# Kernel tuning notes

Measured on AMD Instinct MI355X. Metric: run time of the kernel, lower is better.

## Reference

```python
import jax, jax.numpy as jnp
import numpy as np

B, C, H, W = 8, 256, 56, 56
CI = 64  # inter_channels = C // reduction


def setup_inputs() -> dict:
    key = jax.random.key(0)
    ks = jax.random.split(key, 8)
    s = 0.05
    return {
        "x": jax.random.normal(ks[0], (B, C, H, W), jnp.float32),
        "Wq": jax.random.normal(ks[1], (CI, C), jnp.float32) * s,
        "bq": jax.random.normal(ks[2], (CI,), jnp.float32) * s,
        "Wk": jax.random.normal(ks[3], (CI, C), jnp.float32) * s,
        "bk": jax.random.normal(ks[4], (CI,), jnp.float32) * s,
        "Wv": jax.random.normal(ks[5], (C, C), jnp.float32) * s,
        "bv": jax.random.normal(ks[6], (C,), jnp.float32) * s,
        "gamma": jax.random.normal(ks[7], (1,), jnp.float32) * s,
    }


def reference(x, Wq, bq, Wk, bk, Wv, bv, gamma):
    b, c, h, w = x.shape
    n = h * w
    xf = x.reshape(b, c, n)  # [B, C, N]
    # 1x1 convs == per-pixel linear projections
    q = jnp.einsum('oc,bcn->bno', Wq, xf) + bq          # [B, N, CI]
    k = jnp.einsum('oc,bcn->bon', Wk, xf) + bk[:, None]  # [B, CI, N]
    score = jnp.einsum('bno,bom->bnm', q, k)             # [B, N, N] (no scaling, as in source)
    attention = jax.nn.softmax(score, axis=-1)
    v = jnp.einsum('oc,bcn->bon', Wv, xf) + bv[:, None]  # [B, C, N]
    # out[b,c,i] = sum_j v[b,c,j] * attention[b,i,j]  (== bmm(V, att^T))
    out = jnp.einsum('bcj,bij->bci', v, attention).reshape(b, c, h, w)
    return gamma[0] * out + x
```

## Files before the change

### kernel.cpp

```cpp
#include <hip/hip_runtime.h>


constexpr int B_  = 8;
constexpr int C_  = 256;
constexpr int CI_ = 64;
constexpr int N_  = 3136;
constexpr int JS  = 4;
constexpr int JT  = 32;
constexpr int VSP = 40;
constexpr int PN  = 64;
constexpr int XSP = C_ + 8;

typedef __attribute__((ext_vector_type(8))) short short8;
typedef __attribute__((ext_vector_type(4))) float f32x4;
typedef __attribute__((ext_vector_type(4))) ushort us4;

static __device__ inline ushort f2b(float f) {
    unsigned u = __float_as_uint(f);
    return (ushort)((u + 0x7fffu + ((u >> 16) & 1u)) >> 16);
}
static __device__ inline float b2f(ushort h) {
    return __uint_as_float(((unsigned)h) << 16);
}

__global__ __launch_bounds__(256)
void pre_kernel(const float* __restrict__ x,
                const float* __restrict__ Wq, const float* __restrict__ Wk,
                const float* __restrict__ Wv,
                ushort* __restrict__ xT, ushort* __restrict__ wqk, ushort* __restrict__ wv)
{
    __shared__ float ts[64][65];
    const int bx  = blockIdx.x;
    const int tid = threadIdx.x;

    if (bx >= B_ * 196) {
        int i = (bx - B_ * 196) * 256 + tid;
        if (i < 16384)      wqk[i] = f2b(Wq[i]);
        else if (i < 32768) wqk[i] = f2b(Wk[i - 16384]);
        wv[i] = f2b(Wv[i]);
        return;
    }

    const int b  = bx / 196;
    const int rm = bx % 196;
    const int n0 = (rm >> 2) * 64;
    const int c0 = (rm & 3) * 64;

    const float* src = x + ((size_t)b * C_ + c0) * N_ + n0;
    #pragma unroll
    for (int rep = 0; rep < 16; rep++) {
        int e = rep * 256 + tid;
        int c = e >> 6, n = e & 63;
        ts[c][n] = src[(size_t)c * N_ + n];
    }
    __syncthreads();
    ushort* dst = xT + ((size_t)b * N_ + n0) * C_ + c0;
    #pragma unroll
    for (int rep = 0; rep < 8; rep++) {
        int e = rep * 256 + tid;
        int n = e >> 5, c2 = (e & 31) * 2;
        ushort2 o;
        o.x = f2b(ts[c2][n]);
        o.y = f2b(ts[c2 + 1][n]);
        *(ushort2*)(dst + (size_t)n * C_ + c2) = o;
    }
}

__global__ __launch_bounds__(256)
void proj_kernel(const ushort* __restrict__ xT, const ushort* __restrict__ wqk,
                 const ushort* __restrict__ wv,
                 const float* __restrict__ bq, const float* __restrict__ bk,
                 const float* __restrict__ bv,
                 ushort* __restrict__ qb, ushort* __restrict__ kb, ushort* __restrict__ vt)
{
    __shared__ ushort xs[PN][XSP];
    const int b   = blockIdx.x / 49;
    const int n0  = (blockIdx.x % 49) * PN;
    const int tid = threadIdx.x;
    const int w    = tid >> 6;
    const int lane = tid & 63;
    const int m16  = lane & 15;
    const int quad = lane >> 4;

    {
        const ushort* src = xT + ((size_t)b * N_ + n0) * C_;
        #pragma unroll
        for (int rep = 0; rep < 8; rep++) {
            int e = rep * 256 + tid;
            int row = e >> 5, ch = (e & 31) * 8;
            *(short8*)&xs[row][ch] = *(const short8*)(src + (size_t)row * C_ + ch);
        }
    }
    __syncthreads();

    {
        f32x4 acc[2][4];
        #pragma unroll
        for (int mt = 0; mt < 2; mt++)
            #pragma unroll
            for (int nt = 0; nt < 4; nt++) acc[mt][nt] = (f32x4){0.f, 0.f, 0.f, 0.f};

        #pragma unroll
        for (int kk = 0; kk < 8; kk++) {
            short8 af[2];
            #pragma unroll
            for (int mt = 0; mt < 2; mt++)
                af[mt] = *(const short8*)(wqk + (size_t)(w * 32 + mt * 16 + m16) * C_ + kk * 32 + quad * 8);
            #pragma unroll
            for (int nt = 0; nt < 4; nt++) {
                short8 bf = *(const short8*)&xs[nt * 16 + m16][kk * 32 + quad * 8];
                #pragma unroll
                for (int mt = 0; mt < 2; mt++)
                    acc[mt][nt] = __builtin_amdgcn_mfma_f32_16x16x32_bf16(af[mt], bf, acc[mt][nt], 0, 0, 0);
            }
        }
        const float* bias = (w < 2) ? bq : bk;
        ushort* dst = (w < 2) ? qb : kb;
        const int obase = (w & 1) * 32;
        #pragma unroll
        for (int mt = 0; mt < 2; mt++) {
            f32x4 bs = *(const f32x4*)(bias + obase + mt * 16 + quad * 4);
            #pragma unroll
            for (int nt = 0; nt < 4; nt++) {
                us4 pk;
                pk.x = f2b(acc[mt][nt][0] + bs[0]);
                pk.y = f2b(acc[mt][nt][1] + bs[1]);
                pk.z = f2b(acc[mt][nt][2] + bs[2]);
                pk.w = f2b(acc[mt][nt][3] + bs[3]);
                *(us4*)(dst + ((size_t)b * N_ + n0 + nt * 16 + m16) * CI_ + obase + mt * 16 + quad * 4) = pk;
            }
        }
    }

    {
        f32x4 vacc[4][4];
        #pragma unroll
        for (int mt = 0; mt < 4; mt++)
            #pragma unroll
            for (int nt = 0; nt < 4; nt++) vacc[mt][nt] = (f32x4){0.f, 0.f, 0.f, 0.f};

        #pragma unroll
        for (int kk = 0; kk < 8; kk++) {
            short8 af[4];
            #pragma unroll
            for (int mt = 0; mt < 4; mt++)
                af[mt] = *(const short8*)&xs[mt * 16 + m16][kk * 32 + quad * 8];
            #pragma unroll
            for (int nt = 0; nt < 4; nt++) {
                short8 bf = *(const short8*)(wv + (size_t)(w * 64 + nt * 16 + m16) * C_ + kk * 32 + quad * 8);
                #pragma unroll
                for (int mt = 0; mt < 4; mt++)
                    vacc[mt][nt] = __builtin_amdgcn_mfma_f32_16x16x32_bf16(af[mt], bf, vacc[mt][nt], 0, 0, 0);
            }
        }
        #pragma unroll
        for (int nt = 0; nt < 4; nt++) {
            int c = w * 64 + nt * 16 + m16;
            float bvc = bv[c];
            #pragma unroll
            for (int mt = 0; mt < 4; mt++) {
                us4 pk;
                pk.x = f2b(vacc[mt][nt][0] + bvc);
                pk.y = f2b(vacc[mt][nt][1] + bvc);
                pk.z = f2b(vacc[mt][nt][2] + bvc);
                pk.w = f2b(vacc[mt][nt][3] + bvc);
                *(us4*)(vt + ((size_t)b * C_ + c) * N_ + n0 + mt * 16 + quad * 4) = pk;
            }
        }
    }
}

__global__ __launch_bounds__(256, 2)
void attn_kernel(const ushort* __restrict__ qb, const ushort* __restrict__ kb,
                 const ushort* __restrict__ vt,
                 ushort* __restrict__ op, float* __restrict__ lp)
{
    __shared__ __align__(16) ushort vs[2][C_][VSP];

    const int bx   = blockIdx.x;
    const int b    = bx & 7;
    const int rem  = bx >> 3;
    const int t    = rem >> 2;
    const int js   = rem & 3;
    const int tid  = threadIdx.x;
    const int w    = tid >> 6;
    const int lane = tid & 63;
    const int m16  = lane & 15;
    const int quad = lane >> 4;
    const int i0   = t * 64 + w * 16;

    const int steps = (js == 0) ? 13 : 12;
    const int jbase = ((js == 0) ? 0 : (1 + 12 * js)) * JT;

    const ushort* vtb = vt + (size_t)b * C_ * N_;
    const ushort* kbb = kb + (size_t)b * N_ * CI_;

    short8 qf[2];
    {
        const ushort* qbase = qb + ((size_t)b * N_ + i0 + m16) * CI_;
        qf[0] = *(const short8*)(qbase + quad * 8);
        qf[1] = *(const short8*)(qbase + 32 + quad * 8);
    }

    f32x4 O[16];
    #pragma unroll
    for (int ct = 0; ct < 16; ct++) O[ct] = (f32x4){0.f, 0.f, 0.f, 0.f};
    float lsum = 0.f;

    const int sc  = tid >> 2;
    const int seg = tid & 3;
    const int p0  = (seg & 1) * 16 + (seg >> 1) * 4;

    short8 prA[4], prB[4];
    short8 krA[4], krB[4];

    #define PREFETCH(PR, J0)                                                   \
        {                                                                      \
            _Pragma("unroll")                                                  \
            for (int p = 0; p < 4; p++)                                        \
                PR[p] = *(const short8*)(vtb + (size_t)(p * 64 + sc) * N_ + (J0) + seg * 8); \
        }
    #define COMMIT(PR, BUF)                                                    \
        {                                                                      \
            _Pragma("unroll")                                                  \
            for (int p = 0; p < 4; p++) {                                      \
                *(us4*)&vs[BUF][p * 64 + sc][p0]     = ((const us4*)&PR[p])[0]; \
                *(us4*)&vs[BUF][p * 64 + sc][p0 + 8] = ((const us4*)&PR[p])[1]; \
            }                                                                  \
        }
    #define KLOAD(J0, KR)                                                      \
        {                                                                      \
            _Pragma("unroll")                                                  \
            for (int h = 0; h < 2; h++) {                                      \
                const ushort* krow = kbb + (size_t)((J0) + h * 16 + m16) * CI_; \
                KR[2 * h]     = *(const short8*)(krow + quad * 8);             \
                KR[2 * h + 1] = *(const short8*)(krow + 32 + quad * 8);        \
            }                                                                  \
        }
    #define BAR()                                                              \
        {                                                                      \
            __builtin_amdgcn_sched_barrier(0);                                 \
            asm volatile("s_waitcnt lgkmcnt(0)");                              \
            __builtin_amdgcn_sched_barrier(0);                                 \
            __builtin_amdgcn_s_barrier();                                      \
            __builtin_amdgcn_sched_barrier(0);                                 \
        }

    PREFETCH(prA, jbase)
    PREFETCH(prB, jbase + JT)
    KLOAD(jbase, krA)
    COMMIT(prA, 0)
    BAR()

    #define STEP(CUR, PRC, PRN, KRC, KRN, ST)                                  \
    {                                                                          \
        const int j0_ = jbase + (ST) * JT;                                     \
        const bool more1_ = (ST) + 1 < steps;                                  \
        if ((ST) + 2 < steps) PREFETCH(PRN, j0_ + 2 * JT)                      \
        if (more1_) KLOAD(j0_ + JT, KRN)                                       \
                      \
        short8 pa;                                                             \
        _Pragma("unroll")                                                      \
        for (int h = 0; h < 2; h++) {                                          \
            f32x4 T = (f32x4){0.f, 0.f, 0.f, 0.f};                             \
            T = __builtin_amdgcn_mfma_f32_16x16x32_bf16(KRC[2 * h],     qf[0], T, 0, 0, 0); \
            T = __builtin_amdgcn_mfma_f32_16x16x32_bf16(KRC[2 * h + 1], qf[1], T, 0, 0, 0); \
            _Pragma("unroll")                                                  \
            for (int r = 0; r < 4; r++) {                                      \
                float pv = __expf(T[r] - 12.0f);             \
                lsum += pv;                                                    \
                pa[h * 4 + r] = (short)f2b(pv);                                \
            }                                                                  \
        }                                                                      \
                             \
        __builtin_amdgcn_s_setprio(1);                                         \
        _Pragma("unroll")                                                      \
        for (int ct = 0; ct < 16; ct++) {                                      \
            short8 vf = *(const short8*)&vs[CUR][ct * 16 + m16][quad * 8];     \
            O[ct] = __builtin_amdgcn_mfma_f32_16x16x32_bf16(pa, vf, O[ct], 0, 0, 0); \
        }                                                                      \
        __builtin_amdgcn_s_setprio(0);                                         \
        if (more1_) {                                                          \
            COMMIT(PRC, (CUR) ^ 1)                                             \
            BAR()                                                              \
        }                                                                      \
    }

    int st = 0;
    for (; st + 2 <= steps; st += 2) {
        STEP(0, prB, prA, krA, krB, st)
        STEP(1, prA, prB, krB, krA, st + 1)
    }
    if (st < steps)
        STEP(0, prB, prA, krA, krB, st)

    {
        float v = lsum;
        v += __shfl_xor(v, 16);
        v += __shfl_xor(v, 32);
        if (lane < 16)
            __builtin_nontemporal_store(v, &lp[(size_t)(b * JS + js) * N_ + i0 + lane]);
    }

    ushort* opb = op + (size_t)(b * JS + js) * C_ * N_;
    #pragma unroll
    for (int ct = 0; ct < 16; ct++) {
        us4 pk;
        pk.x = f2b(O[ct][0]);
        pk.y = f2b(O[ct][1]);
        pk.z = f2b(O[ct][2]);
        pk.w = f2b(O[ct][3]);
        __builtin_nontemporal_store(pk,
            (us4*)(opb + (size_t)(ct * 16 + m16) * N_ + i0 + quad * 4));
    }
    #undef PREFETCH
    #undef COMMIT
    #undef KLOAD
    #undef BAR
    #undef STEP
}

__global__ __launch_bounds__(256)
void reduce_kernel(const ushort* __restrict__ op, const float* __restrict__ lp,
                   const float* __restrict__ x, const float* __restrict__ gamma_p,
                   float* __restrict__ out)
{
    const int g  = blockIdx.x * 256 + threadIdx.x;
    const int i4 = g % (N_ / 4);
    const int c  = (g / (N_ / 4)) % C_;
    const int b  = g / ((N_ / 4) * C_);
    const size_t io = (size_t)i4 * 4;
    const float g0 = gamma_p[0];

    f32x4 acc = (f32x4){0.f, 0.f, 0.f, 0.f};
    f32x4 lt  = (f32x4){0.f, 0.f, 0.f, 0.f};
    #pragma unroll
    for (int js = 0; js < JS; js++) {
        us4 a = *(const us4*)(op + ((size_t)(b * JS + js) * C_ + c) * N_ + io);
        f32x4   l = *(const f32x4*)(lp + (size_t)(b * JS + js) * N_ + io);
        acc[0] += b2f(a.x); acc[1] += b2f(a.y); acc[2] += b2f(a.z); acc[3] += b2f(a.w);
        lt += l;
    }

    const size_t xo = ((size_t)b * C_ + c) * N_ + io;
    f32x4 xv = *(const f32x4*)(x + xo);
    f32x4 ov;
    #pragma unroll
    for (int u = 0; u < 4; u++) ov[u] = acc[u] * (g0 / lt[u]) + xv[u];
    *(f32x4*)(out + xo) = ov;
}

extern "C" void kernel_launch(void* const* d_in, const int* in_sizes, int n_in,
                              void* d_out, int out_size, void* d_ws, size_t ws_size,
                              hipStream_t stream)
{
    const float* x  = (const float*)d_in[0];
    const float* Wq = (const float*)d_in[1];
    const float* bq = (const float*)d_in[2];
    const float* Wk = (const float*)d_in[3];
    const float* bk = (const float*)d_in[4];
    const float* Wv = (const float*)d_in[5];
    const float* bv = (const float*)d_in[6];
    const float* gm = (const float*)d_in[7];
    float* out = (float*)d_out;

    ushort* qb   = (ushort*)d_ws;
    ushort* kb   = qb + (size_t)B_ * N_ * CI_;
    ushort* vt   = kb + (size_t)B_ * N_ * CI_;
    ushort* xT   = vt + (size_t)B_ * C_ * N_;
    ushort* wqk  = xT + (size_t)B_ * N_ * C_;
    ushort* wv   = wqk + 128 * C_;
    ushort* op   = wv + 256 * C_;
    float*  lpf  = (float*)(op + (size_t)B_ * JS * C_ * N_);

    hipLaunchKernelGGL(pre_kernel, dim3(B_ * 196 + 256), dim3(256), 0, stream,
                       x, Wq, Wk, Wv, xT, wqk, wv);
    hipLaunchKernelGGL(proj_kernel, dim3(B_ * 49), dim3(256), 0, stream,
                       xT, wqk, wv, bq, bk, bv, qb, kb, vt);
    hipLaunchKernelGGL(attn_kernel, dim3(B_ * 49 * JS), dim3(256), 0, stream,
                       qb, kb, vt, op, lpf);
    hipLaunchKernelGGL(reduce_kernel, dim3(B_ * C_ * (N_ / 4) / 256), dim3(256), 0, stream,
                       op, lpf, x, gm, out);
}
```

Measured before the change: 210.3 us.

## Issue attention tile loads via inline asm with explicit vmcnt waits

The V and K tile loads in the attention kernel become inline-asm global_load_dwordx4 instructions. Each step now waits with an explicit s_waitcnt vmcnt count sized to the number of loads still in flight, instead of relying on the compiler's conservative waits. The step loop is fully unrolled for the 13- or 12-step cases, and the Q loads also move to inline asm. The launch_bounds minimum of two blocks per CU is dropped, so the compiler may use more registers, which risks lower occupancy. The hand-counted vmcnt values must stay exact or the kernel reads data before it arrives.

New measurement: 204.3 us. 1.03x faster.

```diff
diff --git a/kernel.cpp b/kernel.cpp
--- a/kernel.cpp
+++ b/kernel.cpp
@@ -170,7 +170,7 @@
     }
 }
 
-__global__ __launch_bounds__(256, 2)
+__global__ __launch_bounds__(256)
 void attn_kernel(const ushort* __restrict__ qb, const ushort* __restrict__ kb,
                  const ushort* __restrict__ vt,
                  ushort* __restrict__ op, float* __restrict__ lp)
@@ -189,18 +189,10 @@
     const int quad = lane >> 4;
     const int i0   = t * 64 + w * 16;
 
-    const int steps = (js == 0) ? 13 : 12;
     const int jbase = ((js == 0) ? 0 : (1 + 12 * js)) * JT;
 
     const ushort* vtb = vt + (size_t)b * C_ * N_;
     const ushort* kbb = kb + (size_t)b * N_ * CI_;
-
-    short8 qf[2];
-    {
-        const ushort* qbase = qb + ((size_t)b * N_ + i0 + m16) * CI_;
-        qf[0] = *(const short8*)(qbase + quad * 8);
-        qf[1] = *(const short8*)(qbase + 32 + quad * 8);
-    }
 
     f32x4 O[16];
     #pragma unroll
@@ -211,14 +203,36 @@
     const int seg = tid & 3;
     const int p0  = (seg & 1) * 16 + (seg >> 1) * 4;
 
-    short8 prA[4], prB[4];
-    short8 krA[4], krB[4];
-
-    #define PREFETCH(PR, J0)                                                   \
+    const ushort* vbase[4];
+    #pragma unroll
+    for (int p = 0; p < 4; p++)
+        vbase[p] = vtb + (size_t)(p * 64 + sc) * N_ + seg * 8;
+
+    short8 qf[2];
+    short8 pr[2][4];
+    short8 kr[2][4];
+
+    #define GLOAD(DST, ADDR)                                                   \
+        asm volatile("global_load_dwordx4 %0, %1, off"                         \
+                     : "=v"(DST) : "v"(ADDR));
+    #define GPREFETCH(PR, J0)                                                  \
         {                                                                      \
             _Pragma("unroll")                                                  \
-            for (int p = 0; p < 4; p++)                                        \
-                PR[p] = *(const short8*)(vtb + (size_t)(p * 64 + sc) * N_ + (J0) + seg * 8); \
+            for (int p = 0; p < 4; p++) {                                      \
+                const ushort* a_ = vbase[p] + (J0);                            \
+                GLOAD(PR[p], a_)                                               \
+            }                                                                  \
+        }
+    #define GKLOAD(J0, KR)                                                     \
+        {                                                                      \
+            _Pragma("unroll")                                                  \
+            for (int h = 0; h < 2; h++) {                                      \
+                const ushort* krow = kbb + (size_t)((J0) + h * 16 + m16) * CI_; \
+                const ushort* a0_ = krow + quad * 8;                           \
+                const ushort* a1_ = krow + 32 + quad * 8;                      \
+                GLOAD(KR[2 * h], a0_)                                          \
+                GLOAD(KR[2 * h + 1], a1_)                                      \
+            }                                                                  \
         }
     #define COMMIT(PR, BUF)                                                    \
         {                                                                      \
@@ -228,71 +242,77 @@
                 *(us4*)&vs[BUF][p * 64 + sc][p0 + 8] = ((const us4*)&PR[p])[1]; \
             }                                                                  \
         }
-    #define KLOAD(J0, KR)                                                      \
-        {                                                                      \
-            _Pragma("unroll")                                                  \
-            for (int h = 0; h < 2; h++) {                                      \
-                const ushort* krow = kbb + (size_t)((J0) + h * 16 + m16) * CI_; \
-                KR[2 * h]     = *(const short8*)(krow + quad * 8);             \
-                KR[2 * h + 1] = *(const short8*)(krow + 32 + quad * 8);        \
-            }                                                                  \
+    #define VWAIT(N)                                                           \
+        {                                                                      \
+            asm volatile("s_waitcnt vmcnt(" #N ")" ::: "memory");              \
+            __builtin_amdgcn_sched_barrier(0);                                 \
         }
     #define BAR()                                                              \
         {                                                                      \
             __builtin_amdgcn_sched_barrier(0);                                 \
-            asm volatile("s_waitcnt lgkmcnt(0)");                              \
+            asm volatile("s_waitcnt lgkmcnt(0)" ::: "memory");                 \
             __builtin_amdgcn_sched_barrier(0);                                 \
             __builtin_amdgcn_s_barrier();                                      \
             __builtin_amdgcn_sched_barrier(0);                                 \
         }
-
-    PREFETCH(prA, jbase)
-    PREFETCH(prB, jbase + JT)
-    KLOAD(jbase, krA)
-    COMMIT(prA, 0)
+    #define COMPUTE(CUR, KRC)                                                  \
+        {                                                                      \
+            short8 pa;                                                         \
+            _Pragma("unroll")                                                  \
+            for (int h = 0; h < 2; h++) {                                      \
+                f32x4 T = (f32x4){0.f, 0.f, 0.f, 0.f};                         \
+                T = __builtin_amdgcn_mfma_f32_16x16x32_bf16(KRC[2 * h],     qf[0], T, 0, 0, 0); \
+                T = __builtin_amdgcn_mfma_f32_16x16x32_bf16(KRC[2 * h + 1], qf[1], T, 0, 0, 0); \
+                _Pragma("unroll")                                              \
+                for (int r = 0; r < 4; r++) {                                  \
+                    float pv = __expf(T[r] - 12.0f);         \
+                    lsum += pv;                                                \
+                    pa[h * 4 + r] = (short)f2b(pv);                            \
+                }                                                              \
+            }                                                                  \
+            __builtin_amdgcn_s_setprio(1);                                     \
+            _Pragma("unroll")                                                  \
+            for (int ct = 0; ct < 16; ct++) {                                  \
+                short8 vf = *(const short8*)&vs[CUR][ct * 16 + m16][quad * 8]; \
+                O[ct] = __builtin_amdgcn_mfma_f32_16x16x32_bf16(pa, vf, O[ct], 0, 0, 0); \
+            }                                                                  \
+            __builtin_amdgcn_s_setprio(0);                                     \
+        }
+
+    {
+        const ushort* qbase = qb + ((size_t)b * N_ + i0 + m16) * CI_;
+        const ushort* qa0 = qbase + quad * 8;
+        const ushort* qa1 = qbase + 32 + quad * 8;
+        GLOAD(qf[0], qa0)
+        GLOAD(qf[1], qa1)
+        VWAIT(0)
+    }
+    GPREFETCH(pr[0], jbase)
+    GPREFETCH(pr[1], jbase + JT)
+    GKLOAD(jbase, kr[0])
+    VWAIT(8)
+    COMMIT(pr[0], 0)
     BAR()
 
-    #define STEP(CUR, PRC, PRN, KRC, KRN, ST)                                  \
-    {                                                                          \
-        const int j0_ = jbase + (ST) * JT;                                     \
-        const bool more1_ = (ST) + 1 < steps;                                  \
-        if ((ST) + 2 < steps) PREFETCH(PRN, j0_ + 2 * JT)                      \
-        if (more1_) KLOAD(j0_ + JT, KRN)                                       \
-                      \
-        short8 pa;                                                             \
+    #define RUN(STEPS_)                                                        \
         _Pragma("unroll")                                                      \
-        for (int h = 0; h < 2; h++) {                                          \
-            f32x4 T = (f32x4){0.f, 0.f, 0.f, 0.f};                             \
-            T = __builtin_amdgcn_mfma_f32_16x16x32_bf16(KRC[2 * h],     qf[0], T, 0, 0, 0); \
-            T = __builtin_amdgcn_mfma_f32_16x16x32_bf16(KRC[2 * h + 1], qf[1], T, 0, 0, 0); \
-            _Pragma("unroll")                                                  \
-            for (int r = 0; r < 4; r++) {                                      \
-                float pv = __expf(T[r] - 12.0f);             \
-                lsum += pv;                                                    \
-                pa[h * 4 + r] = (short)f2b(pv);                                \
-            }                                                                  \
-        }                                                                      \
-                             \
-        __builtin_amdgcn_s_setprio(1);                                         \
-        _Pragma("unroll")                                                      \
-        for (int ct = 0; ct < 16; ct++) {                                      \
-            short8 vf = *(const short8*)&vs[CUR][ct * 16 + m16][quad * 8];     \
-            O[ct] = __builtin_amdgcn_mfma_f32_16x16x32_bf16(pa, vf, O[ct], 0, 0, 0); \
-        }                                                                      \
-        __builtin_amdgcn_s_setprio(0);                                         \
-        if (more1_) {                                                          \
-            COMMIT(PRC, (CUR) ^ 1)                                             \
-            BAR()                                                              \
-        }                                                                      \
-    }
-
-    int st = 0;
-    for (; st + 2 <= steps; st += 2) {
-        STEP(0, prB, prA, krA, krB, st)
-        STEP(1, prA, prB, krB, krA, st + 1)
-    }
-    if (st < steps)
-        STEP(0, prB, prA, krA, krB, st)
+        for (int st = 0; st < (STEPS_); ++st) {                                \
+            const int cur = st & 1;                                            \
+            const int j0_ = jbase + st * JT;                                   \
+            if (st + 2 < (STEPS_)) GPREFETCH(pr[cur], j0_ + 2 * JT)            \
+            if (st + 1 < (STEPS_)) GKLOAD(j0_ + JT, kr[cur ^ 1])               \
+            if (st + 2 < (STEPS_)) { VWAIT(8) }                                \
+            else if (st + 1 < (STEPS_)) { VWAIT(4) }                           \
+            else { VWAIT(0) }                                                  \
+            COMPUTE(cur, kr[cur])                                              \
+            if (st + 1 < (STEPS_)) {                                           \
+                COMMIT(pr[cur ^ 1], cur ^ 1)                                   \
+                BAR()                                                          \
+            }                                                                  \
+        }
+
+    if (js == 0) { RUN(13) } else { RUN(12) }
+    #undef RUN
 
     {
         float v = lsum;
@@ -313,11 +333,13 @@
         __builtin_nontemporal_store(pk,
             (us4*)(opb + (size_t)(ct * 16 + m16) * N_ + i0 + quad * 4));
     }
-    #undef PREFETCH
+    #undef GLOAD
+    #undef GPREFETCH
+    #undef GKLOAD
     #undef COMMIT
-    #undef KLOAD
+    #undef VWAIT
     #undef BAR
-    #undef STEP
+    #undef COMPUTE
 }
 
 __global__ __launch_bounds__(256)
```
